# Optimization experiments

Hardware: AMD Instinct MI355X
Metric: run time of the kernel (lower is better)

Reference implementation:

```python
import jax, jax.numpy as jnp
import numpy as np

D, H, L, DFF, V = 512, 8, 6, 2048, 32000
PAD = 0

def make_pe(max_len, d):
    pos = jnp.arange(max_len, dtype=jnp.float32)[:, None]
    div = jnp.exp(jnp.arange(0, d, 2, dtype=jnp.float32) * (-np.log(10000.0) / d))
    ang = pos * div  # [max_len, d/2]
    pe = jnp.zeros((max_len, d), jnp.float32)
    pe = pe.at[:, 0::2].set(jnp.sin(ang)).at[:, 1::2].set(jnp.cos(ang))
    return pe

def layernorm(x, g, b, eps=1e-5):
    m = x.mean(-1, keepdims=True)
    v = ((x - m) ** 2).mean(-1, keepdims=True)
    return (x - m) * jax.lax.rsqrt(v + eps) * g + b

def mha(q_in, k_in, v_in, W, Bv, mask):
    # W: [4, D, D] (q,k,v,out); Bv: [4, D]; mask broadcastable to [B,H,Tq,Tk] bool
    b, sq, d = q_in.shape
    hd = d // H
    def proj(x, w, bb):
        y = x @ w + bb
        return y.reshape(x.shape[0], x.shape[1], H, hd).transpose(0, 2, 1, 3)  # bhsd
    Q, K, Vh = proj(q_in, W[0], Bv[0]), proj(k_in, W[1], Bv[1]), proj(v_in, W[2], Bv[2])
    scores = jnp.einsum('bhqd,bhkd->bhqk', Q, K) / np.sqrt(hd).astype(np.float32)
    scores = jnp.where(mask, scores, jnp.float32(-1e9))
    attn = jax.nn.softmax(scores, axis=-1)
    ctx = jnp.einsum('bhqk,bhkd->bhqd', attn, Vh).transpose(0, 2, 1, 3).reshape(b, sq, d)
    return ctx @ W[3] + Bv[3]

def ffn(x, w1, b1, w2, b2):
    return jax.nn.relu(x @ w1 + b1) @ w2 + b2

def setup_inputs() -> dict:
    key = jax.random.key(0)
    ks = jax.random.split(key, 16)
    s = 0.02
    inp = {
        'src': jax.random.randint(ks[0], (8, 512), 0, V, dtype=jnp.int32),
        'tgt': jax.random.randint(ks[1], (8, 512), 0, V, dtype=jnp.int32),
        'src_emb': (jax.random.normal(ks[2], (V, D)) * s).at[PAD].set(0.0),
        'tgt_emb': (jax.random.normal(ks[3], (V, D)) * s).at[PAD].set(0.0),
        'enc_attn_w': jax.random.normal(ks[4], (L, 4, D, D)) * s,
        'enc_attn_b': jnp.zeros((L, 4, D)),
        'enc_ffn_w1': jax.random.normal(ks[5], (L, D, DFF)) * s,
        'enc_ffn_b1': jnp.zeros((L, DFF)),
        'enc_ffn_w2': jax.random.normal(ks[6], (L, DFF, D)) * s,
        'enc_ffn_b2': jnp.zeros((L, D)),
        'enc_ln_g': jnp.ones((L, 2, D)),
        'enc_ln_b': jnp.zeros((L, 2, D)),
        'dec_self_w': jax.random.normal(ks[7], (L, 4, D, D)) * s,
        'dec_self_b': jnp.zeros((L, 4, D)),
        'dec_cross_w': jax.random.normal(ks[8], (L, 4, D, D)) * s,
        'dec_cross_b': jnp.zeros((L, 4, D)),
        'dec_ffn_w1': jax.random.normal(ks[9], (L, D, DFF)) * s,
        'dec_ffn_b1': jnp.zeros((L, DFF)),
        'dec_ffn_w2': jax.random.normal(ks[10], (L, DFF, D)) * s,
        'dec_ffn_b2': jnp.zeros((L, D)),
        'dec_ln_g': jnp.ones((L, 3, D)),
        'dec_ln_b': jnp.zeros((L, 3, D)),
        'out_w': jax.random.normal(ks[11], (D, V)) * s,
        'out_b': jnp.zeros((V,)),
    }
    return inp

def reference(src, tgt, src_emb, tgt_emb, enc_attn_w, enc_attn_b, enc_ffn_w1, enc_ffn_b1,
              enc_ffn_w2, enc_ffn_b2, enc_ln_g, enc_ln_b, dec_self_w, dec_self_b,
              dec_cross_w, dec_cross_b, dec_ffn_w1, dec_ffn_b1, dec_ffn_w2, dec_ffn_b2,
              dec_ln_g, dec_ln_b, out_w, out_b):
    B_, S = src.shape
    T = tgt.shape[1]
    pe = make_pe(max(S, T), D)
    scale = jnp.float32(np.sqrt(D))

    src_pad = (src != PAD)[:, None, None, :]                    # [B,1,1,S]
    causal = jnp.tril(jnp.ones((T, T), bool))                   # [T,T]
    tgt_mask = (tgt != PAD)[:, None, None, :] & causal[None, None]  # [B,1,T,T]

    # encoder (dropout = identity at inference)
    x = src_emb[src] * scale + pe[None, :S]
    for i in range(L):
        a = mha(x, x, x, enc_attn_w[i], enc_attn_b[i], src_pad)
        x = layernorm(x + a, enc_ln_g[i, 0], enc_ln_b[i, 0])
        f = ffn(x, enc_ffn_w1[i], enc_ffn_b1[i], enc_ffn_w2[i], enc_ffn_b2[i])
        x = layernorm(x + f, enc_ln_g[i, 1], enc_ln_b[i, 1])
    memory = x

    # decoder
    y = tgt_emb[tgt] * scale + pe[None, :T]
    for i in range(L):
        a = mha(y, y, y, dec_self_w[i], dec_self_b[i], tgt_mask)
        y = layernorm(y + a, dec_ln_g[i, 0], dec_ln_b[i, 0])
        c = mha(y, memory, memory, dec_cross_w[i], dec_cross_b[i], src_pad)
        y = layernorm(y + c, dec_ln_g[i, 1], dec_ln_b[i, 1])
        f = ffn(y, dec_ffn_w1[i], dec_ffn_b1[i], dec_ffn_w2[i], dec_ffn_b2[i])
        y = layernorm(y + f, dec_ln_g[i, 2], dec_ln_b[i, 2])

    return y @ out_w + out_b  # [B, T, tgt_vocab]
```

## Files before the change

kernel.cpp:

```cpp
#include <hip/hip_runtime.h>
#include <hip/hip_bf16.h>


#define Dm 512
#define Hh 8
#define HD 64
#define Ll 6
#define DFFv 2048
#define Vv 32000
#define Bb 8
#define Ss 512
#define NTOK (Bb * Ss)

typedef __bf16 bf16x8 __attribute__((ext_vector_type(8)));
typedef __bf16 bf16x4 __attribute__((ext_vector_type(4)));
typedef float  f32x4  __attribute__((ext_vector_type(4)));

#define GLOAD16(gp, lp) __builtin_amdgcn_global_load_lds( \
    (const __attribute__((address_space(1))) unsigned int*)(const void*)(gp), \
    (__attribute__((address_space(3))) unsigned int*)(void*)(lp), 16, 0, 0)

__global__ void embed_pe_k(const int* __restrict__ tok, const float* __restrict__ emb,
                           float* __restrict__ out, __bf16* __restrict__ outb, int Slen)
{
    int row = blockIdx.x;
    int s = row % Slen;
    int t = tok[row];
    const float* e = emb + (size_t)t * Dm;
    float* o = out + (size_t)row * Dm;
    __bf16* ob = outb + (size_t)row * Dm;
    for (int dd = threadIdx.x; dd < Dm; dd += blockDim.x) {
        int j = dd >> 1;
        float div = expf((float)(2 * j) * (-9.210340371976184f / 512.0f));
        float ang = (float)s * div;
        float pe = (dd & 1) ? cosf(ang) : sinf(ang);
        float v = e[dd] * 22.627416997969522f + pe;
        o[dd] = v;
        ob[dd] = (__bf16)v;
    }
}

__global__ __launch_bounds__(256) void wtr_k(const float* __restrict__ W,
                                             __bf16* __restrict__ Wt, int K, int N)
{
    __shared__ float t[32][33];
    size_t msz = (size_t)K * N;
    const float* Wm = W + (size_t)blockIdx.z * msz;
    __bf16* Wtm = Wt + (size_t)blockIdx.z * msz;
    int n0 = blockIdx.x * 32, k0 = blockIdx.y * 32;
    int r = threadIdx.x >> 3, c4 = (threadIdx.x & 7) * 4;
    float4 v = *reinterpret_cast<const float4*>(&Wm[(size_t)(k0 + r) * N + n0 + c4]);
    t[r][c4] = v.x; t[r][c4 + 1] = v.y; t[r][c4 + 2] = v.z; t[r][c4 + 3] = v.w;
    __syncthreads();
    int n = threadIdx.x >> 3, kq = (threadIdx.x & 7) * 4;
    bf16x4 o;
    o[0] = (__bf16)t[kq + 0][n]; o[1] = (__bf16)t[kq + 1][n];
    o[2] = (__bf16)t[kq + 2][n]; o[3] = (__bf16)t[kq + 3][n];
    *reinterpret_cast<bf16x4*>(&Wtm[(size_t)(n0 + n) * K + k0 + kq]) = o;
}

template<int BM, int BN, int RELU, int MODE>
__global__ __launch_bounds__(256) void gemm_mfma_k(const __bf16* __restrict__ A,
                                                   const __bf16* __restrict__ Wt,
                                                   const float* __restrict__ bias,
                                                   void* __restrict__ Cout,
                                                   __bf16* __restrict__ out_k,
                                                   __bf16* __restrict__ out_vT,
                                                   int M, int N, int K)
{
    constexpr int NF_M = BM / 32;
    constexpr int NF_N = BN / 32;
    __shared__ __bf16 As[2][BM * 64];
    __shared__ __bf16 Bs[2][BN * 64];
    const int tid = threadIdx.x;
    const int wave = tid >> 6, lane = tid & 63;
    const int wr = wave >> 1, wc = wave & 1;
    const int row0 = blockIdx.y * BM, col0 = blockIdx.x * BN;

    f32x4 acc[NF_M][NF_N] = {};

    const int fr = lane & 15;
    const int kg = lane >> 4;

    auto stage = [&](int buf, int k0) {
        #pragma unroll
        for (int cc = 0; cc < BM / 32; ++cc) {
            int g = cc * 256 + tid;
            int r = g >> 3, cs = g & 7, gs = cs ^ (r & 7);
            GLOAD16(A + (size_t)(row0 + r) * K + k0 + gs * 8, &As[buf][g * 8]);
        }
        #pragma unroll
        for (int cc = 0; cc < BN / 32; ++cc) {
            int g = cc * 256 + tid;
            int r = g >> 3, cs = g & 7, gs = cs ^ (r & 7);
            GLOAD16(Wt + (size_t)(col0 + r) * K + k0 + gs * 8, &Bs[buf][g * 8]);
        }
    };

    stage(0, 0);
    __syncthreads();

    const int nk = K >> 6;
    for (int kb = 0; kb < nk; ++kb) {
        int cur = kb & 1;
        if (kb + 1 < nk) stage(cur ^ 1, (kb + 1) * 64);

        const char* Ab = (const char*)As[cur];
        const char* Bbp = (const char*)Bs[cur];
        #pragma unroll
        for (int ks = 0; ks < 2; ++ks) {
            bf16x8 af[NF_M], bq[NF_N];
            #pragma unroll
            for (int m = 0; m < NF_M; ++m) {
                int ar = wr * (BM / 2) + m * 16 + fr;
                af[m] = *reinterpret_cast<const bf16x8*>(
                    Ab + ar * 128 + (((ks * 4 + kg) ^ (ar & 7)) << 4));
            }
            #pragma unroll
            for (int n = 0; n < NF_N; ++n) {
                int br = wc * (BN / 2) + n * 16 + fr;
                bq[n] = *reinterpret_cast<const bf16x8*>(
                    Bbp + br * 128 + (((ks * 4 + kg) ^ (br & 7)) << 4));
            }
            #pragma unroll
            for (int m = 0; m < NF_M; ++m)
                #pragma unroll
                for (int n = 0; n < NF_N; ++n)
                    acc[m][n] = __builtin_amdgcn_mfma_f32_16x16x32_bf16(
                        af[m], bq[n], acc[m][n], 0, 0, 0);
        }
        __syncthreads();
    }

    #pragma unroll
    for (int m = 0; m < NF_M; ++m) {
        #pragma unroll
        for (int n = 0; n < NF_N; ++n) {
            int colg = col0 + wc * (BN / 2) + n * 16 + fr;
            float bv = bias[colg];
            #pragma unroll
            for (int j = 0; j < 4; ++j) {
                int row = row0 + wr * (BM / 2) + m * 16 + kg * 4 + j;
                float v = acc[m][n][j] + bv;
                if (RELU) v = fmaxf(v, 0.f);
                if constexpr (MODE == 0) {
                    ((float*)Cout)[(size_t)row * N + colg] = v;
                } else if constexpr (MODE == 1) {
                    ((__bf16*)Cout)[(size_t)row * N + colg] = (__bf16)v;
                } else {
                    int seg = colg >> 9;
                    int c = colg & 511;
                    bool isV = (MODE == 2) ? (seg == 2) : (seg == 1);
                    if (!isV) {
                        __bf16* o = (MODE == 2 && seg == 1) ? out_k : (__bf16*)Cout;
                        o[(size_t)row * 512 + c] = (__bf16)v;
                    } else {
                        int bi = row >> 9, s = row & 511;
                        int hh = c >> 6, f = c & 63;
                        out_vT[(size_t)((bi * 8 + hh) * 64 + f) * 512 + s] = (__bf16)v;
                    }
                }
            }
        }
    }
}

__global__ __launch_bounds__(512) void gemm256_k(const __bf16* __restrict__ A,
                                                 const __bf16* __restrict__ Wt,
                                                 const float* __restrict__ bias,
                                                 float* __restrict__ C,
                                                 int M, int N, int K)
{
    __shared__ __bf16 As[2][256 * 64];
    __shared__ __bf16 Bs[2][256 * 64];
    const int tid = threadIdx.x;
    const int wave = tid >> 6, lane = tid & 63;
    const int wr = wave >> 2, wc = wave & 3;
    const int row0 = blockIdx.x * 256, col0 = blockIdx.y * 256;

    f32x4 acc[8][4] = {};

    const int fr = lane & 15;
    const int kg = lane >> 4;

    auto stage = [&](int buf, int k0) {
        #pragma unroll
        for (int cc = 0; cc < 4; ++cc) {
            int g = cc * 512 + tid;
            int r = g >> 3, cs = g & 7, gs = cs ^ (r & 7);
            GLOAD16(A + (size_t)(row0 + r) * K + k0 + gs * 8, &As[buf][g * 8]);
        }
        #pragma unroll
        for (int cc = 0; cc < 4; ++cc) {
            int g = cc * 512 + tid;
            int r = g >> 3, cs = g & 7, gs = cs ^ (r & 7);
            GLOAD16(Wt + (size_t)(col0 + r) * K + k0 + gs * 8, &Bs[buf][g * 8]);
        }
    };

    stage(0, 0);
    __syncthreads();

    const int nk = K >> 6;
    for (int kb = 0; kb < nk; ++kb) {
        int cur = kb & 1;
        if (kb + 1 < nk) stage(cur ^ 1, (kb + 1) * 64);

        const char* Ab = (const char*)As[cur];
        const char* Bbp = (const char*)Bs[cur];
        #pragma unroll
        for (int ks = 0; ks < 2; ++ks) {
            bf16x8 af[8], bq[4];
            #pragma unroll
            for (int m = 0; m < 8; ++m) {
                int ar = wr * 128 + m * 16 + fr;
                af[m] = *reinterpret_cast<const bf16x8*>(
                    Ab + ar * 128 + (((ks * 4 + kg) ^ (ar & 7)) << 4));
            }
            #pragma unroll
            for (int n = 0; n < 4; ++n) {
                int br = wc * 64 + n * 16 + fr;
                bq[n] = *reinterpret_cast<const bf16x8*>(
                    Bbp + br * 128 + (((ks * 4 + kg) ^ (br & 7)) << 4));
            }
            #pragma unroll
            for (int m = 0; m < 8; ++m)
                #pragma unroll
                for (int n = 0; n < 4; ++n)
                    acc[m][n] = __builtin_amdgcn_mfma_f32_16x16x32_bf16(
                        af[m], bq[n], acc[m][n], 0, 0, 0);
        }
        __syncthreads();
    }

    #pragma unroll
    for (int m = 0; m < 8; ++m) {
        #pragma unroll
        for (int n = 0; n < 4; ++n) {
            int colg = col0 + wc * 64 + n * 16 + fr;
            float bv = bias[colg];
            #pragma unroll
            for (int j = 0; j < 4; ++j) {
                int row = row0 + wr * 128 + m * 16 + kg * 4 + j;
                C[(size_t)row * N + colg] = acc[m][n][j] + bv;
            }
        }
    }
}

__global__ __launch_bounds__(256) void attn_mfma_k(const __bf16* __restrict__ Qb,
                                                   const __bf16* __restrict__ Kb,
                                                   const __bf16* __restrict__ VbT,
                                                   __bf16* __restrict__ Ob,
                                                   const int* __restrict__ key_tok,
                                                   int causal)
{
    __shared__ __bf16 Ks[2][128 * 64];
    __shared__ __bf16 Vs[2][64 * 128];
    __shared__ __bf16 Pl[4][16 * 128];

    const int tid = threadIdx.x;
    const int w = tid >> 6, lane = tid & 63;
    const int fr = lane & 15, kg = lane >> 4;
    const int q0 = blockIdx.x * 64;
    const int h = blockIdx.y, b = blockIdx.z;
    const int qrow = q0 + w * 16 + fr;
    const int swz = (fr & 7) << 4;

    bf16x8 qf[2];
    {
        const __bf16* qp = Qb + ((size_t)(b * 512 + qrow) * 512 + h * 64 + kg * 8);
        qf[0] = *reinterpret_cast<const bf16x8*>(qp);
        qf[1] = *reinterpret_cast<const bf16x8*>(qp + 32);
    }

    f32x4 po[4] = {};
    float m_run = -3.0e38f, l_run = 0.f;
    __bf16* pw = Pl[w];

    auto stage = [&](int buf, int kk0) {
        #pragma unroll
        for (int c = 0; c < 4; ++c) {
            int ch = c * 256 + tid;
            int r = ch >> 3, gsk = (ch & 7) ^ (r & 7);
            GLOAD16(Kb + ((size_t)(b * 512 + kk0 + r) * 512 + h * 64 + gsk * 8),
                    &Ks[buf][ch * 8]);
            int f = ch >> 4, gsv = (ch & 15) ^ (f & 7);
            GLOAD16(VbT + ((size_t)((b * 8 + h) * 64 + f) * 512 + kk0 + gsv * 8),
                    &Vs[buf][ch * 8]);
        }
    };

    const int kkend = causal ? ((q0 + 64 + 127) & ~127) : 512;
    stage(0, 0);
    __syncthreads();

    for (int kk0 = 0; kk0 < kkend; kk0 += 128) {
        int cur = (kk0 >> 7) & 1;
        if (kk0 + 128 < kkend) stage(cur ^ 1, kk0 + 128);

        unsigned long long vm0 = __ballot(key_tok[b * 512 + kk0 + lane] != 0);
        unsigned long long vm1 = __ballot(key_tok[b * 512 + kk0 + 64 + lane] != 0);

        f32x4 st[8];
        #pragma unroll
        for (int kt = 0; kt < 8; ++kt) {
            f32x4 s = {};
            #pragma unroll
            for (int ks = 0; ks < 2; ++ks) {
                int byte = ((kt * 16 + fr) * 128 + ks * 64 + kg * 16) ^ swz;
                bf16x8 kf = *reinterpret_cast<const bf16x8*>((const char*)Ks[cur] + byte);
                s = __builtin_amdgcn_mfma_f32_16x16x32_bf16(kf, qf[ks], s, 0, 0, 0);
            }
            st[kt] = s;
        }

        float sv[8][4];
        float mloc = -3.0e38f;
        #pragma unroll
        for (int kt = 0; kt < 8; ++kt) {
            unsigned long long vm = (kt < 4) ? vm0 : vm1;
            #pragma unroll
            for (int j = 0; j < 4; ++j) {
                int kl = kt * 16 + kg * 4 + j;
                float s = st[kt][j] * 0.125f;
                bool ok = (vm >> (kl & 63)) & 1ull;
                if (causal && (kk0 + kl > qrow)) ok = false;
                s = ok ? s : -1e9f;
                sv[kt][j] = s;
                mloc = fmaxf(mloc, s);
            }
        }
        mloc = fmaxf(mloc, __shfl_xor(mloc, 16));
        mloc = fmaxf(mloc, __shfl_xor(mloc, 32));
        float m_new = fmaxf(m_run, mloc);
        float scale = __expf(m_run - m_new);
        float ls = 0.f;
        #pragma unroll
        for (int kt = 0; kt < 8; ++kt)
            #pragma unroll
            for (int j = 0; j < 4; ++j) {
                float p = __expf(sv[kt][j] - m_new);
                sv[kt][j] = p;
                ls += p;
            }
        ls += __shfl_xor(ls, 16);
        ls += __shfl_xor(ls, 32);
        l_run = l_run * scale + ls;
        m_run = m_new;

        #pragma unroll
        for (int kt = 0; kt < 8; ++kt)
            #pragma unroll
            for (int c = 0; c < 2; ++c) {
                union { __bf16 hh[2]; unsigned u; } pk;
                pk.hh[0] = (__bf16)sv[kt][2 * c];
                pk.hh[1] = (__bf16)sv[kt][2 * c + 1];
                int byte = (fr * 256 + kt * 32 + kg * 8 + c * 4) ^ swz;
                *reinterpret_cast<unsigned*>((char*)pw + byte) = pk.u;
            }

        {
            int qb4 = kg * 4;
            float s0 = __shfl(scale, qb4 + 0), s1 = __shfl(scale, qb4 + 1);
            float s2 = __shfl(scale, qb4 + 2), s3 = __shfl(scale, qb4 + 3);
            #pragma unroll
            for (int nf = 0; nf < 4; ++nf) {
                po[nf][0] *= s0; po[nf][1] *= s1;
                po[nf][2] *= s2; po[nf][3] *= s3;
            }
        }

        #pragma unroll
        for (int ks2 = 0; ks2 < 4; ++ks2) {
            int pbyte = (fr * 256 + ks2 * 64 + kg * 16) ^ swz;
            bf16x8 pa = *reinterpret_cast<const bf16x8*>((const char*)pw + pbyte);
            #pragma unroll
            for (int nf = 0; nf < 4; ++nf) {
                int vbyte = ((nf * 16 + fr) * 256 + ks2 * 64 + kg * 16) ^ swz;
                bf16x8 vf = *reinterpret_cast<const bf16x8*>((const char*)Vs[cur] + vbyte);
                po[nf] = __builtin_amdgcn_mfma_f32_16x16x32_bf16(pa, vf, po[nf], 0, 0, 0);
            }
        }
        __syncthreads();
    }

    {
        int qb4 = kg * 4;
        float r0 = 1.0f / __shfl(l_run, qb4 + 0);
        float r1 = 1.0f / __shfl(l_run, qb4 + 1);
        float r2 = 1.0f / __shfl(l_run, qb4 + 2);
        float r3 = 1.0f / __shfl(l_run, qb4 + 3);
        #pragma unroll
        for (int nf = 0; nf < 4; ++nf) {
            size_t base = (size_t)(b * 512 + q0 + w * 16 + qb4) * 512 + h * 64 + nf * 16 + fr;
            Ob[base]           = (__bf16)(po[nf][0] * r0);
            Ob[base + 512]     = (__bf16)(po[nf][1] * r1);
            Ob[base + 1024]    = (__bf16)(po[nf][2] * r2);
            Ob[base + 1536]    = (__bf16)(po[nf][3] * r3);
        }
    }
}

__global__ __launch_bounds__(256) void add_ln_k(float* __restrict__ x,
                                                const float* __restrict__ a,
                                                const float* __restrict__ g,
                                                const float* __restrict__ bb,
                                                __bf16* __restrict__ xb)
{
    int row = blockIdx.x;
    size_t base = (size_t)row * Dm;
    int tid = threadIdx.x;
    float v0 = x[base + tid]       + a[base + tid];
    float v1 = x[base + tid + 256] + a[base + tid + 256];
    float s  = v0 + v1;
    float s2 = v0 * v0 + v1 * v1;
    #pragma unroll
    for (int o = 1; o < 64; o <<= 1) {
        s  += __shfl_xor(s, o);
        s2 += __shfl_xor(s2, o);
    }
    __shared__ float red[8];
    int wid = tid >> 6, lane = tid & 63;
    if (lane == 0) { red[wid] = s; red[wid + 4] = s2; }
    __syncthreads();
    s  = red[0] + red[1] + red[2] + red[3];
    s2 = red[4] + red[5] + red[6] + red[7];
    float mean = s * (1.0f / 512.0f);
    float var  = s2 * (1.0f / 512.0f) - mean * mean;
    float rstd = rsqrtf(var + 1e-5f);
    float y0 = (v0 - mean) * rstd * g[tid]       + bb[tid];
    float y1 = (v1 - mean) * rstd * g[tid + 256] + bb[tid + 256];
    x[base + tid]        = y0;
    x[base + tid + 256]  = y1;
    xb[base + tid]       = (__bf16)y0;
    xb[base + tid + 256] = (__bf16)y1;
}

extern "C" void kernel_launch(void* const* d_in, const int* in_sizes, int n_in,
                              void* d_out, int out_size, void* d_ws, size_t ws_size,
                              hipStream_t stream)
{
    const int*   src        = (const int*)  d_in[0];
    const int*   tgt        = (const int*)  d_in[1];
    const float* src_emb    = (const float*)d_in[2];
    const float* tgt_emb    = (const float*)d_in[3];
    const float* enc_attn_w = (const float*)d_in[4];
    const float* enc_attn_b = (const float*)d_in[5];
    const float* enc_ffn_w1 = (const float*)d_in[6];
    const float* enc_ffn_b1 = (const float*)d_in[7];
    const float* enc_ffn_w2 = (const float*)d_in[8];
    const float* enc_ffn_b2 = (const float*)d_in[9];
    const float* enc_ln_g   = (const float*)d_in[10];
    const float* enc_ln_b   = (const float*)d_in[11];
    const float* dec_self_w = (const float*)d_in[12];
    const float* dec_self_b = (const float*)d_in[13];
    const float* dec_cross_w= (const float*)d_in[14];
    const float* dec_cross_b= (const float*)d_in[15];
    const float* dec_ffn_w1 = (const float*)d_in[16];
    const float* dec_ffn_b1 = (const float*)d_in[17];
    const float* dec_ffn_w2 = (const float*)d_in[18];
    const float* dec_ffn_b2 = (const float*)d_in[19];
    const float* dec_ln_g   = (const float*)d_in[20];
    const float* dec_ln_b   = (const float*)d_in[21];
    const float* out_w      = (const float*)d_in[22];
    const float* out_b      = (const float*)d_in[23];

    const size_t NROW = (size_t)NTOK * Dm;
    const size_t NH1  = (size_t)NTOK * DFFv;

    float* ws  = (float*)d_ws;
    float* xe  = ws;
    float* xd  = xe + NROW;
    float* t0  = xd + NROW;

    __bf16* xeb  = (__bf16*)(t0 + NROW);
    __bf16* xdb  = xeb + NROW;
    __bf16* qbb  = xdb + NROW;
    __bf16* kbb  = qbb + NROW;
    __bf16* vbT  = kbb + NROW;
    __bf16* ctxb = vbT + NROW;
    __bf16* h1b  = ctxb + NROW;

    const size_t WSZ  = (size_t)Dm * Dm;
    const size_t FSZ  = (size_t)Dm * DFFv;
    __bf16* w_enc_attn = h1b + NH1;
    __bf16* w_enc_f1   = w_enc_attn + 24 * WSZ;
    __bf16* w_enc_f2   = w_enc_f1 + 6 * FSZ;
    __bf16* w_dec_self = w_enc_f2 + 6 * FSZ;
    __bf16* w_dec_cross= w_dec_self + 24 * WSZ;
    __bf16* w_dec_f1   = w_dec_cross + 24 * WSZ;
    __bf16* w_dec_f2   = w_dec_f1 + 6 * FSZ;
    __bf16* w_out      = w_dec_f2 + 6 * FSZ;

    wtr_k<<<dim3(Dm / 32, Dm / 32, 24), 256, 0, stream>>>(enc_attn_w, w_enc_attn, Dm, Dm);
    wtr_k<<<dim3(DFFv / 32, Dm / 32, 6), 256, 0, stream>>>(enc_ffn_w1, w_enc_f1, Dm, DFFv);
    wtr_k<<<dim3(Dm / 32, DFFv / 32, 6), 256, 0, stream>>>(enc_ffn_w2, w_enc_f2, DFFv, Dm);
    wtr_k<<<dim3(Dm / 32, Dm / 32, 24), 256, 0, stream>>>(dec_self_w, w_dec_self, Dm, Dm);
    wtr_k<<<dim3(Dm / 32, Dm / 32, 24), 256, 0, stream>>>(dec_cross_w, w_dec_cross, Dm, Dm);
    wtr_k<<<dim3(DFFv / 32, Dm / 32, 6), 256, 0, stream>>>(dec_ffn_w1, w_dec_f1, Dm, DFFv);
    wtr_k<<<dim3(Dm / 32, DFFv / 32, 6), 256, 0, stream>>>(dec_ffn_w2, w_dec_f2, DFFv, Dm);
    wtr_k<<<dim3(Vv / 32, Dm / 32, 1), 256, 0, stream>>>(out_w, w_out, Dm, Vv);

    auto gqkv = [&](const __bf16* A, const __bf16* Wt, const float* bias) {
        gemm_mfma_k<64, 128, 0, 2><<<dim3(1536 / 128, NTOK / 64), 256, 0, stream>>>(
            A, Wt, bias, qbb, kbb, vbT, NTOK, 1536, Dm);
    };
    auto gkv = [&](const __bf16* A, const __bf16* Wt, const float* bias) {
        gemm_mfma_k<64, 128, 0, 3><<<dim3(1024 / 128, NTOK / 64), 256, 0, stream>>>(
            A, Wt, bias, kbb, nullptr, vbT, NTOK, 1024, Dm);
    };
    auto g64f = [&](const __bf16* A, const __bf16* Wt, const float* bias, float* C, int K) {
        gemm_mfma_k<64, 64, 0, 0><<<dim3(Dm / 64, NTOK / 64), 256, 0, stream>>>(
            A, Wt, bias, C, nullptr, nullptr, NTOK, Dm, K);
    };
    auto attn = [&](const __bf16* Q, const __bf16* K, const __bf16* Vt, __bf16* O,
                    const int* kt, int causal) {
        attn_mfma_k<<<dim3(Ss / 64, Hh, Bb), 256, 0, stream>>>(Q, K, Vt, O, kt, causal);
    };
    auto lnorm = [&](float* x, const float* a, const float* g, const float* b, __bf16* xb) {
        add_ln_k<<<NTOK, 256, 0, stream>>>(x, a, g, b, xb);
    };

    embed_pe_k<<<NTOK, 256, 0, stream>>>(src, src_emb, xe, xeb, Ss);
    embed_pe_k<<<NTOK, 256, 0, stream>>>(tgt, tgt_emb, xd, xdb, Ss);

    for (int i = 0; i < Ll; ++i) {
        const __bf16* W = w_enc_attn + (size_t)i * 4 * WSZ;
        const float* Bv = enc_attn_b + (size_t)i * 4 * Dm;
        gqkv(xeb, W, Bv);
        attn(qbb, kbb, vbT, ctxb, src, 0);
        g64f(ctxb, W + 3 * WSZ, Bv + 3 * Dm, t0, Dm);
        lnorm(xe, t0, enc_ln_g + i * 2 * Dm, enc_ln_b + i * 2 * Dm, xeb);
        gemm_mfma_k<128, 128, 1, 1><<<dim3(DFFv / 128, NTOK / 128), 256, 0, stream>>>(
            xeb, w_enc_f1 + (size_t)i * FSZ, enc_ffn_b1 + i * DFFv, h1b, nullptr, nullptr,
            NTOK, DFFv, Dm);
        g64f(h1b, w_enc_f2 + (size_t)i * FSZ, enc_ffn_b2 + i * Dm, t0, DFFv);
        lnorm(xe, t0, enc_ln_g + i * 2 * Dm + Dm, enc_ln_b + i * 2 * Dm + Dm, xeb);
    }

    for (int i = 0; i < Ll; ++i) {
        const __bf16* Wsf = w_dec_self + (size_t)i * 4 * WSZ;
        const float* Bsf = dec_self_b + (size_t)i * 4 * Dm;
        gqkv(xdb, Wsf, Bsf);
        attn(qbb, kbb, vbT, ctxb, tgt, 1);
        g64f(ctxb, Wsf + 3 * WSZ, Bsf + 3 * Dm, t0, Dm);
        lnorm(xd, t0, dec_ln_g + i * 3 * Dm, dec_ln_b + i * 3 * Dm, xdb);

        const __bf16* Wc = w_dec_cross + (size_t)i * 4 * WSZ;
        const float* Bc = dec_cross_b + (size_t)i * 4 * Dm;
        gemm_mfma_k<64, 64, 0, 1><<<dim3(Dm / 64, NTOK / 64), 256, 0, stream>>>(
            xdb, Wc + 0 * WSZ, Bc + 0 * Dm, qbb, nullptr, nullptr, NTOK, Dm, Dm);
        gkv(xeb, Wc + 1 * WSZ, Bc + 1 * Dm);
        attn(qbb, kbb, vbT, ctxb, src, 0);
        g64f(ctxb, Wc + 3 * WSZ, Bc + 3 * Dm, t0, Dm);
        lnorm(xd, t0, dec_ln_g + i * 3 * Dm + Dm, dec_ln_b + i * 3 * Dm + Dm, xdb);

        gemm_mfma_k<128, 128, 1, 1><<<dim3(DFFv / 128, NTOK / 128), 256, 0, stream>>>(
            xdb, w_dec_f1 + (size_t)i * FSZ, dec_ffn_b1 + i * DFFv, h1b, nullptr, nullptr,
            NTOK, DFFv, Dm);
        g64f(h1b, w_dec_f2 + (size_t)i * FSZ, dec_ffn_b2 + i * Dm, t0, DFFv);
        lnorm(xd, t0, dec_ln_g + i * 3 * Dm + 2 * Dm, dec_ln_b + i * 3 * Dm + 2 * Dm, xdb);
    }

    gemm256_k<<<dim3(NTOK / 256, Vv / 256), 512, 0, stream>>>(
        xdb, w_out, out_b, (float*)d_out, NTOK, Vv, Dm);
}
```

Baseline: 2.130 ms.

## Triple-buffer GEMM pipeline, batch cross-attention KV projections, remap output GEMM grid

The generic MFMA GEMM moves from double to triple LDS buffering, with explicit vmcnt waits and raw barriers in place of __syncthreads, and raises wave priority around the MFMA blocks. The decoder's cross-attention K/V projections for all six layers run as one wide GEMM over the encoder memory after the encoder finishes, replacing six smaller launches; this needs extra workspace for six K and V buffers. FFN1 switches to 64x128 tiles. The vocab GEMM uses a 1D grid with an XCD-aware block remap and a restructured inner loop that waits on vmcnt explicitly. The cost is more LDS per block, which may lower occupancy, and hand-written waitcnt logic that is fragile.

```diff
diff --git a/kernel.cpp b/kernel.cpp
--- a/kernel.cpp
+++ b/kernel.cpp
@@ -11,6 +11,7 @@
 #define Bb 8
 #define Ss 512
 #define NTOK (Bb * Ss)
+#define NROWC ((size_t)NTOK * Dm)
 
 typedef __bf16 bf16x8 __attribute__((ext_vector_type(8)));
 typedef __bf16 bf16x4 __attribute__((ext_vector_type(4)));
@@ -19,6 +20,13 @@
 #define GLOAD16(gp, lp) __builtin_amdgcn_global_load_lds( \
     (const __attribute__((address_space(1))) unsigned int*)(const void*)(gp), \
     (__attribute__((address_space(3))) unsigned int*)(void*)(lp), 16, 0, 0)
+
+template<int N> __device__ __forceinline__ void vwait() {
+    if constexpr (N == 0) asm volatile("s_waitcnt vmcnt(0)" ::: "memory");
+    else if constexpr (N == 4) asm volatile("s_waitcnt vmcnt(4)" ::: "memory");
+    else if constexpr (N == 6) asm volatile("s_waitcnt vmcnt(6)" ::: "memory");
+    else if constexpr (N == 8) asm volatile("s_waitcnt vmcnt(8)" ::: "memory");
+}
 
 __global__ void embed_pe_k(const int* __restrict__ tok, const float* __restrict__ emb,
                            float* __restrict__ out, __bf16* __restrict__ outb, int Slen)
@@ -70,43 +78,54 @@
 {
     constexpr int NF_M = BM / 32;
     constexpr int NF_N = BN / 32;
-    __shared__ __bf16 As[2][BM * 64];
-    __shared__ __bf16 Bs[2][BN * 64];
+    constexpr int LPT  = (BM + BN) / 32;
+    __shared__ __bf16 As[3][BM * 64];
+    __shared__ __bf16 Bs[3][BN * 64];
     const int tid = threadIdx.x;
     const int wave = tid >> 6, lane = tid & 63;
     const int wr = wave >> 1, wc = wave & 1;
     const int row0 = blockIdx.y * BM, col0 = blockIdx.x * BN;
 
     f32x4 acc[NF_M][NF_N] = {};
-
     const int fr = lane & 15;
     const int kg = lane >> 4;
 
-    auto stage = [&](int buf, int k0) {
+    auto stage = [&](int slot, int kt) {
+        int k0 = kt << 6;
         #pragma unroll
         for (int cc = 0; cc < BM / 32; ++cc) {
             int g = cc * 256 + tid;
-            int r = g >> 3, cs = g & 7, gs = cs ^ (r & 7);
-            GLOAD16(A + (size_t)(row0 + r) * K + k0 + gs * 8, &As[buf][g * 8]);
+            int r = g >> 3, gs = (g & 7) ^ (r & 7);
+            GLOAD16(A + (size_t)(row0 + r) * K + k0 + gs * 8, &As[slot][g * 8]);
         }
         #pragma unroll
         for (int cc = 0; cc < BN / 32; ++cc) {
             int g = cc * 256 + tid;
-            int r = g >> 3, cs = g & 7, gs = cs ^ (r & 7);
-            GLOAD16(Wt + (size_t)(col0 + r) * K + k0 + gs * 8, &Bs[buf][g * 8]);
-        }
-    };
-
+            int r = g >> 3, gs = (g & 7) ^ (r & 7);
+            int c = col0 + r;
+            size_t wrow;
+            if constexpr (MODE == 4)
+                wrow = (size_t)(c >> 10) * 2048 + 512 + (c & 1023);
+            else
+                wrow = (size_t)c;
+            GLOAD16(Wt + wrow * K + k0 + gs * 8, &Bs[slot][g * 8]);
+        }
+    };
+
+    const int nkt = K >> 6;
     stage(0, 0);
-    __syncthreads();
-
-    const int nk = K >> 6;
-    for (int kb = 0; kb < nk; ++kb) {
-        int cur = kb & 1;
-        if (kb + 1 < nk) stage(cur ^ 1, (kb + 1) * 64);
-
-        const char* Ab = (const char*)As[cur];
-        const char* Bbp = (const char*)Bs[cur];
+    stage(1, 1);
+    vwait<LPT>();
+    __builtin_amdgcn_s_barrier();
+    __builtin_amdgcn_sched_barrier(0);
+
+    for (int t = 0; t < nkt; ++t) {
+        int s = t % 3;
+        bool pf = (t + 2) < nkt;
+        if (pf) stage((t + 2) % 3, t + 2);
+
+        const char* Ab  = (const char*)As[s];
+        const char* Bbp = (const char*)Bs[s];
         #pragma unroll
         for (int ks = 0; ks < 2; ++ks) {
             bf16x8 af[NF_M], bq[NF_N];
@@ -122,14 +141,19 @@
                 bq[n] = *reinterpret_cast<const bf16x8*>(
                     Bbp + br * 128 + (((ks * 4 + kg) ^ (br & 7)) << 4));
             }
+            __builtin_amdgcn_s_setprio(1);
             #pragma unroll
             for (int m = 0; m < NF_M; ++m)
                 #pragma unroll
                 for (int n = 0; n < NF_N; ++n)
                     acc[m][n] = __builtin_amdgcn_mfma_f32_16x16x32_bf16(
                         af[m], bq[n], acc[m][n], 0, 0, 0);
-        }
-        __syncthreads();
+            __builtin_amdgcn_s_setprio(0);
+        }
+        __builtin_amdgcn_sched_barrier(0);
+        if (pf) vwait<LPT>(); else vwait<0>();
+        __builtin_amdgcn_s_barrier();
+        __builtin_amdgcn_sched_barrier(0);
     }
 
     #pragma unroll
@@ -137,7 +161,11 @@
         #pragma unroll
         for (int n = 0; n < NF_N; ++n) {
             int colg = col0 + wc * (BN / 2) + n * 16 + fr;
-            float bv = bias[colg];
+            float bv;
+            if constexpr (MODE == 4)
+                bv = bias[(colg >> 10) * 2048 + 512 + (colg & 1023)];
+            else
+                bv = bias[colg];
             #pragma unroll
             for (int j = 0; j < 4; ++j) {
                 int row = row0 + wr * (BM / 2) + m * 16 + kg * 4 + j;
@@ -147,17 +175,28 @@
                     ((float*)Cout)[(size_t)row * N + colg] = v;
                 } else if constexpr (MODE == 1) {
                     ((__bf16*)Cout)[(size_t)row * N + colg] = (__bf16)v;
-                } else {
+                } else if constexpr (MODE == 2) {
                     int seg = colg >> 9;
                     int c = colg & 511;
-                    bool isV = (MODE == 2) ? (seg == 2) : (seg == 1);
-                    if (!isV) {
-                        __bf16* o = (MODE == 2 && seg == 1) ? out_k : (__bf16*)Cout;
-                        o[(size_t)row * 512 + c] = (__bf16)v;
+                    if (seg == 0) {
+                        ((__bf16*)Cout)[(size_t)row * 512 + c] = (__bf16)v;
+                    } else if (seg == 1) {
+                        out_k[(size_t)row * 512 + c] = (__bf16)v;
                     } else {
-                        int bi = row >> 9, s = row & 511;
+                        int bi = row >> 9, sI = row & 511;
                         int hh = c >> 6, f = c & 63;
-                        out_vT[(size_t)((bi * 8 + hh) * 64 + f) * 512 + s] = (__bf16)v;
+                        out_vT[(size_t)((bi * 8 + hh) * 64 + f) * 512 + sI] = (__bf16)v;
+                    }
+                } else {
+                    int li = colg >> 10;
+                    int cw = colg & 1023;
+                    if (cw < 512) {
+                        out_k[li * NROWC + (size_t)row * 512 + cw] = (__bf16)v;
+                    } else {
+                        int hh = (cw - 512) >> 6, f = (cw - 512) & 63;
+                        int bi = row >> 9, sI = row & 511;
+                        out_vT[li * NROWC +
+                               (size_t)((bi * 8 + hh) * 64 + f) * 512 + sI] = (__bf16)v;
                     }
                 }
             }
@@ -176,61 +215,82 @@
     const int tid = threadIdx.x;
     const int wave = tid >> 6, lane = tid & 63;
     const int wr = wave >> 2, wc = wave & 3;
-    const int row0 = blockIdx.x * 256, col0 = blockIdx.y * 256;
+    const int nwg = gridDim.x;
+    const int xcd = blockIdx.x & 7, lid = blockIdx.x >> 3;
+    const int orig = xcd * (nwg >> 3) + lid;
+    const int row0 = (orig & 15) * 256;
+    const int col0 = (orig >> 4) * 256;
 
     f32x4 acc[8][4] = {};
-
     const int fr = lane & 15;
     const int kg = lane >> 4;
 
-    auto stage = [&](int buf, int k0) {
+    auto stage = [&](int slot, int kt) {
+        int k0 = kt << 6;
         #pragma unroll
         for (int cc = 0; cc < 4; ++cc) {
             int g = cc * 512 + tid;
-            int r = g >> 3, cs = g & 7, gs = cs ^ (r & 7);
-            GLOAD16(A + (size_t)(row0 + r) * K + k0 + gs * 8, &As[buf][g * 8]);
+            int r = g >> 3, gs = (g & 7) ^ (r & 7);
+            GLOAD16(A + (size_t)(row0 + r) * K + k0 + gs * 8, &As[slot][g * 8]);
         }
         #pragma unroll
         for (int cc = 0; cc < 4; ++cc) {
             int g = cc * 512 + tid;
-            int r = g >> 3, cs = g & 7, gs = cs ^ (r & 7);
-            GLOAD16(Wt + (size_t)(col0 + r) * K + k0 + gs * 8, &Bs[buf][g * 8]);
-        }
-    };
-
+            int r = g >> 3, gs = (g & 7) ^ (r & 7);
+            GLOAD16(Wt + (size_t)(col0 + r) * K + k0 + gs * 8, &Bs[slot][g * 8]);
+        }
+    };
+
+    const int nkt = K >> 6;
     stage(0, 0);
-    __syncthreads();
-
-    const int nk = K >> 6;
-    for (int kb = 0; kb < nk; ++kb) {
-        int cur = kb & 1;
-        if (kb + 1 < nk) stage(cur ^ 1, (kb + 1) * 64);
-
-        const char* Ab = (const char*)As[cur];
-        const char* Bbp = (const char*)Bs[cur];
-        #pragma unroll
-        for (int ks = 0; ks < 2; ++ks) {
-            bf16x8 af[8], bq[4];
-            #pragma unroll
-            for (int m = 0; m < 8; ++m) {
-                int ar = wr * 128 + m * 16 + fr;
-                af[m] = *reinterpret_cast<const bf16x8*>(
-                    Ab + ar * 128 + (((ks * 4 + kg) ^ (ar & 7)) << 4));
-            }
-            #pragma unroll
-            for (int n = 0; n < 4; ++n) {
+    stage(1, 1);
+    vwait<8>();
+    __builtin_amdgcn_s_barrier();
+    __builtin_amdgcn_sched_barrier(0);
+
+    for (int t = 0; t < nkt; ++t) {
+        int s = t & 1;
+        bool pf = (t + 2) < nkt;
+        const char* Ab  = (const char*)As[s];
+        const char* Bbp = (const char*)Bs[s];
+
+        bf16x8 bq[4][2];
+        #pragma unroll
+        for (int n = 0; n < 4; ++n)
+            #pragma unroll
+            for (int ks = 0; ks < 2; ++ks) {
                 int br = wc * 64 + n * 16 + fr;
-                bq[n] = *reinterpret_cast<const bf16x8*>(
+                bq[n][ks] = *reinterpret_cast<const bf16x8*>(
                     Bbp + br * 128 + (((ks * 4 + kg) ^ (br & 7)) << 4));
             }
-            #pragma unroll
-            for (int m = 0; m < 8; ++m)
+        #pragma unroll
+        for (int q = 0; q < 4; ++q) {
+            bf16x8 af[2][2];
+            #pragma unroll
+            for (int m2 = 0; m2 < 2; ++m2)
+                #pragma unroll
+                for (int ks = 0; ks < 2; ++ks) {
+                    int ar = wr * 128 + (q * 2 + m2) * 16 + fr;
+                    af[m2][ks] = *reinterpret_cast<const bf16x8*>(
+                        Ab + ar * 128 + (((ks * 4 + kg) ^ (ar & 7)) << 4));
+                }
+            __builtin_amdgcn_s_setprio(1);
+            #pragma unroll
+            for (int m2 = 0; m2 < 2; ++m2)
                 #pragma unroll
                 for (int n = 0; n < 4; ++n)
-                    acc[m][n] = __builtin_amdgcn_mfma_f32_16x16x32_bf16(
-                        af[m], bq[n], acc[m][n], 0, 0, 0);
-        }
-        __syncthreads();
+                    #pragma unroll
+                    for (int ks = 0; ks < 2; ++ks)
+                        acc[q * 2 + m2][n] = __builtin_amdgcn_mfma_f32_16x16x32_bf16(
+                            af[m2][ks], bq[n][ks], acc[q * 2 + m2][n], 0, 0, 0);
+            __builtin_amdgcn_s_setprio(0);
+        }
+        __builtin_amdgcn_sched_barrier(0);
+        __builtin_amdgcn_s_barrier();
+        if (pf) stage(s, t + 2);
+        if (pf) vwait<8>(); else vwait<0>();
+        __builtin_amdgcn_s_barrier();
+        __builtin_amdgcn_sched_barrier(0);
     }
 
     #pragma unroll
@@ -466,7 +526,7 @@
     const float* out_w      = (const float*)d_in[22];
     const float* out_b      = (const float*)d_in[23];
 
-    const size_t NROW = (size_t)NTOK * Dm;
+    const size_t NROW = NROWC;
     const size_t NH1  = (size_t)NTOK * DFFv;
 
     float* ws  = (float*)d_ws;
@@ -481,10 +541,12 @@
     __bf16* vbT  = kbb + NROW;
     __bf16* ctxb = vbT + NROW;
     __bf16* h1b  = ctxb + NROW;
+    __bf16* kbb6 = h1b + NH1;
+    __bf16* vbT6 = kbb6 + 6 * NROW;
 
     const size_t WSZ  = (size_t)Dm * Dm;
     const size_t FSZ  = (size_t)Dm * DFFv;
-    __bf16* w_enc_attn = h1b + NH1;
+    __bf16* w_enc_attn = vbT6 + 6 * NROW;
     __bf16* w_enc_f1   = w_enc_attn + 24 * WSZ;
     __bf16* w_enc_f2   = w_enc_f1 + 6 * FSZ;
     __bf16* w_dec_self = w_enc_f2 + 6 * FSZ;
@@ -506,13 +568,17 @@
         gemm_mfma_k<64, 128, 0, 2><<<dim3(1536 / 128, NTOK / 64), 256, 0, stream>>>(
             A, Wt, bias, qbb, kbb, vbT, NTOK, 1536, Dm);
     };
-    auto gkv = [&](const __bf16* A, const __bf16* Wt, const float* bias) {
-        gemm_mfma_k<64, 128, 0, 3><<<dim3(1024 / 128, NTOK / 64), 256, 0, stream>>>(
-            A, Wt, bias, kbb, nullptr, vbT, NTOK, 1024, Dm);
-    };
     auto g64f = [&](const __bf16* A, const __bf16* Wt, const float* bias, float* C, int K) {
         gemm_mfma_k<64, 64, 0, 0><<<dim3(Dm / 64, NTOK / 64), 256, 0, stream>>>(
             A, Wt, bias, C, nullptr, nullptr, NTOK, Dm, K);
+    };
+    auto g64b = [&](const __bf16* A, const __bf16* Wt, const float* bias, __bf16* C, int K) {
+        gemm_mfma_k<64, 64, 0, 1><<<dim3(Dm / 64, NTOK / 64), 256, 0, stream>>>(
+            A, Wt, bias, C, nullptr, nullptr, NTOK, Dm, K);
+    };
+    auto gffn1 = [&](const __bf16* A, const __bf16* Wt, const float* bias) {
+        gemm_mfma_k<64, 128, 1, 1><<<dim3(DFFv / 128, NTOK / 64), 256, 0, stream>>>(
+            A, Wt, bias, h1b, nullptr, nullptr, NTOK, DFFv, Dm);
     };
     auto attn = [&](const __bf16* Q, const __bf16* K, const __bf16* Vt, __bf16* O,
                     const int* kt, int causal) {
@@ -532,12 +598,13 @@
         attn(qbb, kbb, vbT, ctxb, src, 0);
         g64f(ctxb, W + 3 * WSZ, Bv + 3 * Dm, t0, Dm);
         lnorm(xe, t0, enc_ln_g + i * 2 * Dm, enc_ln_b + i * 2 * Dm, xeb);
-        gemm_mfma_k<128, 128, 1, 1><<<dim3(DFFv / 128, NTOK / 128), 256, 0, stream>>>(
-            xeb, w_enc_f1 + (size_t)i * FSZ, enc_ffn_b1 + i * DFFv, h1b, nullptr, nullptr,
-            NTOK, DFFv, Dm);
+        gffn1(xeb, w_enc_f1 + (size_t)i * FSZ, enc_ffn_b1 + i * DFFv);
         g64f(h1b, w_enc_f2 + (size_t)i * FSZ, enc_ffn_b2 + i * Dm, t0, DFFv);
         lnorm(xe, t0, enc_ln_g + i * 2 * Dm + Dm, enc_ln_b + i * 2 * Dm + Dm, xeb);
     }
+
+    gemm_mfma_k<64, 128, 0, 4><<<dim3(6144 / 128, NTOK / 64), 256, 0, stream>>>(
+        xeb, w_dec_cross, dec_cross_b, nullptr, kbb6, vbT6, NTOK, 6144, Dm);
 
     for (int i = 0; i < Ll; ++i) {
         const __bf16* Wsf = w_dec_self + (size_t)i * 4 * WSZ;
@@ -549,20 +616,15 @@
 
         const __bf16* Wc = w_dec_cross + (size_t)i * 4 * WSZ;
         const float* Bc = dec_cross_b + (size_t)i * 4 * Dm;
-        gemm_mfma_k<64, 64, 0, 1><<<dim3(Dm / 64, NTOK / 64), 256, 0, stream>>>(
-            xdb, Wc + 0 * WSZ, Bc + 0 * Dm, qbb, nullptr, nullptr, NTOK, Dm, Dm);
-        gkv(xeb, Wc + 1 * WSZ, Bc + 1 * Dm);
-        attn(qbb, kbb, vbT, ctxb, src, 0);
+        g64b(xdb, Wc + 0 * WSZ, Bc + 0 * Dm, qbb, Dm);
+        attn(qbb, kbb6 + (size_t)i * NROW, vbT6 + (size_t)i * NROW, ctxb, src, 0);
         g64f(ctxb, Wc + 3 * WSZ, Bc + 3 * Dm, t0, Dm);
         lnorm(xd, t0, dec_ln_g + i * 3 * Dm + Dm, dec_ln_b + i * 3 * Dm + Dm, xdb);
 
-        gemm_mfma_k<128, 128, 1, 1><<<dim3(DFFv / 128, NTOK / 128), 256, 0, stream>>>(
-            xdb, w_dec_f1 + (size_t)i * FSZ, dec_ffn_b1 + i * DFFv, h1b, nullptr, nullptr,
-            NTOK, DFFv, Dm);
+        gffn1(xdb, w_dec_f1 + (size_t)i * FSZ, dec_ffn_b1 + i * DFFv);
         g64f(h1b, w_dec_f2 + (size_t)i * FSZ, dec_ffn_b2 + i * Dm, t0, DFFv);
         lnorm(xd, t0, dec_ln_g + i * 3 * Dm + 2 * Dm, dec_ln_b + i * 3 * Dm + 2 * Dm, xdb);
     }
 
-    gemm256_k<<<dim3(NTOK / 256, Vv / 256), 512, 0, stream>>>(
-        xdb, w_out, out_b, (float*)d_out, NTOK, Vv, Dm);
-}
+    gemm256_k<<<2000, 512, 0, stream>>>(xdb, w_out, out_b, (float*)d_out, NTOK, Vv, Dm);
+}
```

After: 2.267 ms. 1.06x slower.
